# Optimization experiments

Hardware: AMD Instinct MI355X
Metric: run time of the kernel (lower is better)

Reference implementation:

```python
import jax, jax.numpy as jnp
import numpy as np

N_EMBD = 16
HEAD_SIZE = 64
B, T = 8, 4096


def setup_inputs() -> dict:
    key = jax.random.key(0)
    k_x, k_q, k_k, k_v = jax.random.split(key, 4)
    # Uniform(0,1) keeps QK^T scores strictly positive so the fractional
    # power (-1/16) is well-defined (negative base would NaN, same as torch).
    x = jax.random.uniform(k_x, (B, T, N_EMBD), dtype=jnp.float32)
    Wq = jax.random.uniform(k_q, (N_EMBD, HEAD_SIZE), dtype=jnp.float32) * 0.25
    Wk = jax.random.uniform(k_k, (N_EMBD, HEAD_SIZE), dtype=jnp.float32) * 0.25
    Wv = jax.random.uniform(k_v, (N_EMBD, HEAD_SIZE), dtype=jnp.float32) * 0.25
    return {"x": x, "Wq": Wq, "Wk": Wk, "Wv": Wv}


def reference(x, Wq, Wk, Wv):
    features_dim = x.shape[-1]  # n_embd = 16
    q = x @ Wq                                   # [B, T, H]
    k = x @ Wk                                   # [B, T, H]
    scores = jnp.einsum('bth,bsh->bts', q, k)    # [B, T, T]
    scores = scores ** (-1.0 / features_dim)     # elementwise power, NOT a scale
    attn = jax.nn.softmax(scores, axis=1)        # softmax over QUERY axis (dim=1)
    v = x @ Wk                                   # faithful to source: uses keys_matrix, not Wv
    return jnp.einsum('bts,bsh->bth', attn, v)   # [B, T, H]
```

## Files before the change

kernel.cpp:

```cpp
#include <hip/hip_runtime.h>
#include <hip/hip_bf16.h>

#define BB 8
#define TT 4096
#define EE 16
#define HH 64
#define ZT 16
#define NS 8

typedef __attribute__((ext_vector_type(8))) __bf16 bf16x8;
typedef __attribute__((ext_vector_type(4))) __bf16 bf16x4;
typedef __attribute__((ext_vector_type(4))) float f32x4;

static __device__ __forceinline__ float exp_pow16(float d) {
    float t = __builtin_amdgcn_logf(d) - 5.5f;
    float r = __builtin_fmaf(t, 2.72889e-6f, -9.35716e-5f);
    r = __builtin_fmaf(t, r, 2.90736e-3f);
    r = __builtin_fmaf(t, r, -7.50656e-2f);
    r = __builtin_fmaf(t, r, 2.198967f);
    return r;
}

__global__ __launch_bounds__(256) void proj_kernel(
        const float* __restrict__ x, const float* __restrict__ Wq,
        const float* __restrict__ Wk,
        __bf16* __restrict__ Yb, __bf16* __restrict__ xb,
        float* __restrict__ Dsum) {
    __shared__ float Ms[16][16];
    __shared__ float xs[16][16];
    int tid = threadIdx.x;
    size_t gid = (size_t)blockIdx.x * 256 + tid;
    if (gid < (size_t)BB * TT / 4)
        ((float4*)Dsum)[gid] = (float4){0.f, 0.f, 0.f, 0.f};
    int i = tid >> 4, j = tid & 15;
    float m = 0.f;
#pragma unroll 8
    for (int h = 0; h < HH; ++h) m += Wq[i * HH + h] * Wk[j * HH + h];
    Ms[i][j] = m;
    int row0 = blockIdx.x * 16;
    xs[i][j] = x[(size_t)(row0 + i) * EE + j];
    __syncthreads();
    float y = 0.f;
#pragma unroll
    for (int k = 0; k < EE; ++k) y += xs[i][k] * Ms[k][j];
    size_t idx = (size_t)(row0 + i) * EE + j;
    Yb[idx] = (__bf16)y;
    xb[idx] = (__bf16)xs[i][j];
}

__global__ __launch_bounds__(256) void colsum_mfma(
        const __bf16* __restrict__ Yb, const __bf16* __restrict__ xb,
        float* __restrict__ Dsum) {
    int lane = threadIdx.x & 63;
    int w = threadIdx.x >> 6;
    int quad = lane >> 4;
    int l15 = lane & 15;
    int b = blockIdx.y;
    int z = blockIdx.z;
    int s0 = blockIdx.x * 256 + w * 64;

    const __bf16* xbb = xb + (size_t)b * TT * EE;
    const __bf16* Ybb = Yb + (size_t)b * TT * EE;

    bf16x8 bx[4];
#pragma unroll
    for (int st = 0; st < 4; ++st) {
        bf16x8 v = {};
        if (quad < 2)
            v = *(const bf16x8*)(xbb + (size_t)(s0 + st * 16 + l15) * EE + quad * 8);
        bx[st] = v;
    }

    const int TL = TT / ZT;
    int t0 = z * TL, tend = t0 + TL;

    float csum[4] = {0.f, 0.f, 0.f, 0.f};
    for (int t = t0; t < tend; t += 32) {
        bf16x8 ya[2];
#pragma unroll
        for (int ts = 0; ts < 2; ++ts) {
            bf16x8 v = {};
            if (quad < 2)
                v = *(const bf16x8*)(Ybb + (size_t)(t + ts * 16 + l15) * EE + quad * 8);
            ya[ts] = v;
        }
#pragma unroll
        for (int st = 0; st < 4; ++st) {
#pragma unroll
            for (int ts = 0; ts < 2; ++ts) {
                f32x4 c = {0.f, 0.f, 0.f, 0.f};
                c = __builtin_amdgcn_mfma_f32_16x16x32_bf16(ya[ts], bx[st], c, 0, 0, 0);
                csum[st] += exp_pow16(c[0]) + exp_pow16(c[1])
                          + exp_pow16(c[2]) + exp_pow16(c[3]);
            }
        }
    }

#pragma unroll
    for (int st = 0; st < 4; ++st) {
        float r = csum[st];
        r += __shfl_xor(r, 16, 64);
        r += __shfl_xor(r, 32, 64);
        if (quad == 0)
            atomicAdd(&Dsum[(size_t)b * TT + s0 + st * 16 + l15], r);
    }
}

__global__ __launch_bounds__(256) void xd_kernel(
        const __bf16* __restrict__ xb, const float* __restrict__ Dsum,
        __bf16* __restrict__ xDT, float* __restrict__ Z) {
    __shared__ float Rs[64];
    __shared__ __bf16 tt[16][68];
    int b = blockIdx.y;
    int s0 = blockIdx.x * 64;
    int tid = threadIdx.x;
    size_t zi = ((size_t)b * gridDim.x + blockIdx.x) * 256 + tid;
    ((float4*)Z)[zi] = (float4){0.f, 0.f, 0.f, 0.f};
    if (tid < 64)
        Rs[tid] = 1.0f / Dsum[(size_t)b * TT + s0 + tid];
    __syncthreads();
    int sl = tid & 63, eg = tid >> 6;
    bf16x4 v = *(const bf16x4*)(xb + ((size_t)b * TT + s0 + sl) * EE + eg * 4);
    float r = Rs[sl];
#pragma unroll
    for (int i = 0; i < 4; ++i) tt[eg * 4 + i][sl] = (__bf16)((float)v[i] * r);
    __syncthreads();
    int e = tid >> 4, sc = tid & 15;
    *(bf16x4*)(xDT + ((size_t)b * EE + e) * TT + s0 + sc * 4) = *(const bf16x4*)&tt[e][sc * 4];
}

__global__ __launch_bounds__(256) void out_mfma(
        const __bf16* __restrict__ Yb, const __bf16* __restrict__ xb,
        const __bf16* __restrict__ xDT, float* __restrict__ Z) {
    __shared__ __bf16 Etile[4][2][16 * 40];

    int lane = threadIdx.x & 63;
    int w = threadIdx.x >> 6;
    int quad = lane >> 4;
    int l15 = lane & 15;
    int b = blockIdx.y;
    int z = blockIdx.z;
    int t0 = blockIdx.x * 128 + w * 32;

    const __bf16* xbb = xb + (size_t)b * TT * EE;
    const __bf16* Ybb = Yb + (size_t)b * TT * EE;
    const __bf16* xdb = xDT + (size_t)b * EE * TT;

    bf16x8 yf[2];
#pragma unroll
    for (int tile = 0; tile < 2; ++tile) {
        bf16x8 v = {};
        if (quad < 2)
            v = *(const bf16x8*)(Ybb + (size_t)(t0 + tile * 16 + l15) * EE + quad * 8);
        yf[tile] = v;
    }

    f32x4 acc[2] = {{0.f, 0.f, 0.f, 0.f}, {0.f, 0.f, 0.f, 0.f}};

    const int SL = TT / NS;
    int s0z = z * SL, send = s0z + SL;

    for (int s = s0z; s < send; s += 32) {
        bf16x8 af[2];
#pragma unroll
        for (int ss = 0; ss < 2; ++ss) {
            bf16x8 v = {};
            if (quad < 2)
                v = *(const bf16x8*)(xbb + (size_t)(s + ss * 16 + l15) * EE + quad * 8);
            af[ss] = v;
        }
        bf16x8 bxd = *(const bf16x8*)(xdb + (size_t)l15 * TT + s + quad * 8);

#pragma unroll
        for (int tile = 0; tile < 2; ++tile) {
#pragma unroll
            for (int ss = 0; ss < 2; ++ss) {
                f32x4 c = {0.f, 0.f, 0.f, 0.f};
                c = __builtin_amdgcn_mfma_f32_16x16x32_bf16(af[ss], yf[tile], c, 0, 0, 0);
                bf16x4 e;
#pragma unroll
                for (int r = 0; r < 4; ++r)
                    e[r] = (__bf16)exp_pow16(c[r]);
                *(bf16x4*)&Etile[w][tile][l15 * 40 + ss * 16 + quad * 4] = e;
            }
        }
#pragma unroll
        for (int tile = 0; tile < 2; ++tile) {
            bf16x8 aE = *(const bf16x8*)&Etile[w][tile][l15 * 40 + quad * 8];
            acc[tile] = __builtin_amdgcn_mfma_f32_16x16x32_bf16(aE, bxd, acc[tile], 0, 0, 0);
        }
    }

    float* zp = Z + ((size_t)b * TT + t0) * EE;
#pragma unroll
    for (int tile = 0; tile < 2; ++tile)
#pragma unroll
        for (int r = 0; r < 4; ++r)
            atomicAdd(&zp[(size_t)(tile * 16 + quad * 4 + r) * EE + l15], acc[tile][r]);
}

__global__ __launch_bounds__(256) void zout_kernel(
        const float* __restrict__ Z, const float* __restrict__ Wk,
        float* __restrict__ out) {
    __shared__ float zs[64][16];
    int b = blockIdx.y;
    int t0 = blockIdx.x * 64;
    int tid = threadIdx.x;
    ((float4*)zs)[tid] = ((const float4*)(Z + ((size_t)b * TT + t0) * EE))[tid];
    __syncthreads();
    int h = tid & 63, tg = tid >> 6;
    float wcol[16];
#pragma unroll
    for (int e = 0; e < EE; ++e) wcol[e] = Wk[e * HH + h];
    float* ob = out + ((size_t)b * TT + t0) * HH + h;
#pragma unroll
    for (int k = 0; k < 16; ++k) {
        int tl = tg * 16 + k;
        float o = 0.f;
#pragma unroll
        for (int e = 0; e < EE; ++e) o = __builtin_fmaf(zs[tl][e], wcol[e], o);
        ob[(size_t)tl * HH] = o;
    }
}

extern "C" void kernel_launch(void* const* d_in, const int* in_sizes, int n_in,
                              void* d_out, int out_size, void* d_ws, size_t ws_size,
                              hipStream_t stream) {
    const float* x  = (const float*)d_in[0];
    const float* Wq = (const float*)d_in[1];
    const float* Wk = (const float*)d_in[2];

    const size_t NE16 = (size_t)BB * TT * EE;
    char* wp = (char*)d_ws;
    __bf16* Yb   = (__bf16*)wp;  wp += NE16 * 2;
    __bf16* xbb  = (__bf16*)wp;  wp += NE16 * 2;
    __bf16* xDT  = (__bf16*)wp;  wp += NE16 * 2;
    float*  Dsum = (float*)wp;   wp += (size_t)BB * TT * 4;
    float*  Zws  = (float*)wp;

    float* out = (float*)d_out;

    proj_kernel<<<BB * TT / 16, 256, 0, stream>>>(x, Wq, Wk, Yb, xbb, Dsum);
    colsum_mfma<<<dim3(TT / 256, BB, ZT), 256, 0, stream>>>(Yb, xbb, Dsum);
    xd_kernel<<<dim3(TT / 64, BB), 256, 0, stream>>>(xbb, Dsum, xDT, Zws);
    out_mfma<<<dim3(TT / 128, BB, NS), 256, 0, stream>>>(Yb, xbb, xDT, Zws);
    zout_kernel<<<dim3(TT / 64, BB), 256, 0, stream>>>(Zws, Wk, out);
}
```

Baseline: 153.9 us.

## Software-pipeline colsum and out kernels with double-buffered loads, fold polynomial shift

Rewrites the exp_pow16 polynomial to take log(d) directly, dropping one subtract per element. Both MFMA kernels now double-buffer their global loads so the next chunk's fragments are fetched while the current chunk's MFMA and polynomial work runs. out_mfma now handles one 16-row query tile per wave instead of two and launches twice as many blocks, with a ping-pong LDS buffer for the E tile. This trades reuse of the xb and xDT loads across tiles for more parallelism and overlap, and raises register pressure from the extra buffers.

```diff
diff --git a/kernel.cpp b/kernel.cpp
--- a/kernel.cpp
+++ b/kernel.cpp
@@ -13,11 +13,11 @@
 typedef __attribute__((ext_vector_type(4))) float f32x4;
 
 static __device__ __forceinline__ float exp_pow16(float d) {
-    float t = __builtin_amdgcn_logf(d) - 5.5f;
-    float r = __builtin_fmaf(t, 2.72889e-6f, -9.35716e-5f);
-    r = __builtin_fmaf(t, r, 2.90736e-3f);
-    r = __builtin_fmaf(t, r, -7.50656e-2f);
-    r = __builtin_fmaf(t, r, 2.198967f);
+    float L = __builtin_amdgcn_logf(d);
+    float r = __builtin_fmaf(L, 2.72889e-6f, -1.536072e-4f);
+    r = __builtin_fmaf(L, r, 4.946584e-3f);
+    r = __builtin_fmaf(L, r, -0.11735442f);
+    r = __builtin_fmaf(L, r, 2.71784054f);
     return r;
 }
 
@@ -75,8 +75,8 @@
     int t0 = z * TL, tend = t0 + TL;
 
     float csum[4] = {0.f, 0.f, 0.f, 0.f};
-    for (int t = t0; t < tend; t += 32) {
-        bf16x8 ya[2];
+
+    auto LOADY = [&](bf16x8 ya[2], int t) {
 #pragma unroll
         for (int ts = 0; ts < 2; ++ts) {
             bf16x8 v = {};
@@ -84,6 +84,8 @@
                 v = *(const bf16x8*)(Ybb + (size_t)(t + ts * 16 + l15) * EE + quad * 8);
             ya[ts] = v;
         }
+    };
+    auto BODY = [&](bf16x8 ya[2]) {
 #pragma unroll
         for (int st = 0; st < 4; ++st) {
 #pragma unroll
@@ -94,6 +96,16 @@
                           + exp_pow16(c[2]) + exp_pow16(c[3]);
             }
         }
+    };
+
+    bf16x8 yaA[2], yaB[2];
+    LOADY(yaA, t0);
+    for (int t = t0; t < tend; t += 64) {
+        LOADY(yaB, t + 32);
+        BODY(yaA);
+        int tn = (t + 64 < tend) ? (t + 64) : t0;
+        LOADY(yaA, tn);
+        BODY(yaB);
     }
 
 #pragma unroll
@@ -132,7 +144,7 @@
 __global__ __launch_bounds__(256) void out_mfma(
         const __bf16* __restrict__ Yb, const __bf16* __restrict__ xb,
         const __bf16* __restrict__ xDT, float* __restrict__ Z) {
-    __shared__ __bf16 Etile[4][2][16 * 40];
+    __shared__ __bf16 Etile[2][4][16 * 40];
 
     int lane = threadIdx.x & 63;
     int w = threadIdx.x >> 6;
@@ -140,28 +152,22 @@
     int l15 = lane & 15;
     int b = blockIdx.y;
     int z = blockIdx.z;
-    int t0 = blockIdx.x * 128 + w * 32;
+    int t0 = blockIdx.x * 64 + w * 16;
 
     const __bf16* xbb = xb + (size_t)b * TT * EE;
     const __bf16* Ybb = Yb + (size_t)b * TT * EE;
     const __bf16* xdb = xDT + (size_t)b * EE * TT;
 
-    bf16x8 yf[2];
-#pragma unroll
-    for (int tile = 0; tile < 2; ++tile) {
-        bf16x8 v = {};
-        if (quad < 2)
-            v = *(const bf16x8*)(Ybb + (size_t)(t0 + tile * 16 + l15) * EE + quad * 8);
-        yf[tile] = v;
-    }
-
-    f32x4 acc[2] = {{0.f, 0.f, 0.f, 0.f}, {0.f, 0.f, 0.f, 0.f}};
+    bf16x8 yf = {};
+    if (quad < 2)
+        yf = *(const bf16x8*)(Ybb + (size_t)(t0 + l15) * EE + quad * 8);
+
+    f32x4 acc = {0.f, 0.f, 0.f, 0.f};
 
     const int SL = TT / NS;
     int s0z = z * SL, send = s0z + SL;
 
-    for (int s = s0z; s < send; s += 32) {
-        bf16x8 af[2];
+    auto LOADF = [&](bf16x8 af[2], bf16x8& bxd, int s) {
 #pragma unroll
         for (int ss = 0; ss < 2; ++ss) {
             bf16x8 v = {};
@@ -169,34 +175,44 @@
                 v = *(const bf16x8*)(xbb + (size_t)(s + ss * 16 + l15) * EE + quad * 8);
             af[ss] = v;
         }
-        bf16x8 bxd = *(const bf16x8*)(xdb + (size_t)l15 * TT + s + quad * 8);
-
-#pragma unroll
-        for (int tile = 0; tile < 2; ++tile) {
-#pragma unroll
-            for (int ss = 0; ss < 2; ++ss) {
-                f32x4 c = {0.f, 0.f, 0.f, 0.f};
-                c = __builtin_amdgcn_mfma_f32_16x16x32_bf16(af[ss], yf[tile], c, 0, 0, 0);
-                bf16x4 e;
-#pragma unroll
-                for (int r = 0; r < 4; ++r)
-                    e[r] = (__bf16)exp_pow16(c[r]);
-                *(bf16x4*)&Etile[w][tile][l15 * 40 + ss * 16 + quad * 4] = e;
-            }
-        }
-#pragma unroll
-        for (int tile = 0; tile < 2; ++tile) {
-            bf16x8 aE = *(const bf16x8*)&Etile[w][tile][l15 * 40 + quad * 8];
-            acc[tile] = __builtin_amdgcn_mfma_f32_16x16x32_bf16(aE, bxd, acc[tile], 0, 0, 0);
-        }
+        bxd = *(const bf16x8*)(xdb + (size_t)l15 * TT + s + quad * 8);
+    };
+    auto STAGE = [&](bf16x8 af[2], int p) {
+#pragma unroll
+        for (int ss = 0; ss < 2; ++ss) {
+            f32x4 c = {0.f, 0.f, 0.f, 0.f};
+            c = __builtin_amdgcn_mfma_f32_16x16x32_bf16(af[ss], yf, c, 0, 0, 0);
+            bf16x4 e;
+#pragma unroll
+            for (int r = 0; r < 4; ++r)
+                e[r] = (__bf16)exp_pow16(c[r]);
+            *(bf16x4*)&Etile[p][w][l15 * 40 + ss * 16 + quad * 4] = e;
+        }
+    };
+    auto PV = [&](bf16x8& bxd, int p) {
+        bf16x8 aE = *(const bf16x8*)&Etile[p][w][l15 * 40 + quad * 8];
+        acc = __builtin_amdgcn_mfma_f32_16x16x32_bf16(aE, bxd, acc, 0, 0, 0);
+    };
+
+    bf16x8 afA[2], afB[2], bxdA, bxdB;
+    LOADF(afA, bxdA, s0z);
+    STAGE(afA, 0);
+    for (int s = s0z; s < send; s += 64) {
+        LOADF(afB, bxdB, s + 32);
+        STAGE(afB, 1);
+        PV(bxdA, 0);
+        int sn = s + 64;
+        if (sn < send) {
+            LOADF(afA, bxdA, sn);
+            STAGE(afA, 0);
+        }
+        PV(bxdB, 1);
     }
 
     float* zp = Z + ((size_t)b * TT + t0) * EE;
 #pragma unroll
-    for (int tile = 0; tile < 2; ++tile)
-#pragma unroll
-        for (int r = 0; r < 4; ++r)
-            atomicAdd(&zp[(size_t)(tile * 16 + quad * 4 + r) * EE + l15], acc[tile][r]);
+    for (int r = 0; r < 4; ++r)
+        atomicAdd(&zp[(size_t)(quad * 4 + r) * EE + l15], acc[r]);
 }
 
 __global__ __launch_bounds__(256) void zout_kernel(
@@ -243,6 +259,6 @@
     proj_kernel<<<BB * TT / 16, 256, 0, stream>>>(x, Wq, Wk, Yb, xbb, Dsum);
     colsum_mfma<<<dim3(TT / 256, BB, ZT), 256, 0, stream>>>(Yb, xbb, Dsum);
     xd_kernel<<<dim3(TT / 64, BB), 256, 0, stream>>>(xbb, Dsum, xDT, Zws);
-    out_mfma<<<dim3(TT / 128, BB, NS), 256, 0, stream>>>(Yb, xbb, xDT, Zws);
+    out_mfma<<<dim3(TT / 64, BB, NS), 256, 0, stream>>>(Yb, xbb, xDT, Zws);
     zout_kernel<<<dim3(TT / 64, BB), 256, 0, stream>>>(Zws, Wk, out);
 }
```

Result: slower. 164.2 us (+6.7%).
